# Optimization experiments

Measured on AMD Instinct MI355X. Metric: run time of the kernel, lower is better.

Reference implementation:

```python
import jax, jax.numpy as jnp
import numpy as np

NUM_USERS = 100000
NUM_ITEMS = 50000
DIM = 64
N_LAYERS = 3
L_W = 1e-4
E0 = 600000          # raw user-item interactions
B = 8192             # BPR batch size
N_NODES = NUM_USERS + NUM_ITEMS


def setup_inputs() -> dict:
    key = jax.random.key(0)
    k1, k2, k3, k4, k5, k6, k7 = jax.random.split(key, 7)
    return {
        "Gu": jax.random.normal(k1, (NUM_USERS, DIM), jnp.float32) * 0.1,
        "Gi": jax.random.normal(k2, (NUM_ITEMS, DIM), jnp.float32) * 0.1,
        "edge_user": jax.random.randint(k3, (E0,), 0, NUM_USERS),
        "edge_item": jax.random.randint(k4, (E0,), 0, NUM_ITEMS),
        "user": jax.random.randint(k5, (B,), 0, NUM_USERS),
        "pos": jax.random.randint(k6, (B,), 0, NUM_ITEMS),
        "neg": jax.random.randint(k7, (B,), 0, NUM_ITEMS),
    }


def _propagate(Gu, Gi, src, dst):
    # symmetric normalized adjacency (gcn_norm, no self-loops, as in LGConv)
    deg = jax.ops.segment_sum(jnp.ones_like(src, jnp.float32), dst,
                              num_segments=N_NODES)
    dinv = jnp.where(deg > 0, jax.lax.rsqrt(deg), 0.0)
    w = dinv[src] * dinv[dst]                      # [E]
    x = jnp.concatenate([Gu, Gi], axis=0)          # [N, D]
    acc = x
    h = x
    for _ in range(N_LAYERS):
        # SpMM: h' = D^-1/2 A D^-1/2 h  (gather + weighted scatter-add)
        h = jax.ops.segment_sum(w[:, None] * h[src], dst,
                                num_segments=N_NODES)
        acc = acc + h
    emb = acc / (N_LAYERS + 1)                     # mean over all layers
    return emb[:NUM_USERS], emb[NUM_USERS:]


def reference(Gu, Gi, edge_user, edge_item, user, pos, neg):
    # symmetrize bipartite edges; items offset by NUM_USERS
    src = jnp.concatenate([edge_user, edge_item + NUM_USERS])
    dst = jnp.concatenate([edge_item + NUM_USERS, edge_user])
    gu, gi = _propagate(Gu, Gi, src, dst)
    gu_u, gi_p, gi_n = gu[user], gi[pos], gi[neg]  # [B, D]
    xu_pos = jnp.sum(gu_u * gi_p, axis=1)
    xu_neg = jnp.sum(gu_u * gi_n, axis=1)
    mf_loss = -jnp.mean(jax.nn.log_sigmoid(xu_pos - xu_neg))
    reg = L_W * 0.5 * (jnp.sum(gu_u ** 2) + jnp.sum(gi_p ** 2)
                       + jnp.sum(gi_n ** 2)) / B
    return mf_loss + reg
```

## Files before the change

### kernel.cpp

```cpp
#include <hip/hip_runtime.h>

#define NUSERS 100000
#define NITEMS 50000
#define NNODES 150000
#define DIM 64
#define E0 600000
#define E2 (2 * E0)
#define BB 8192
#define LW 1e-4f
#define NN16 150016
#define LOSS_BLOCKS 512
#define SPMM_B 2344
#define SPMMB_B 384

#define NBUCK 1172
#define CHUNK_E 2048
#define CHUNKS 293
#define CPAD 320
#define BCAP 3072

__device__ __forceinline__ float bf_lo(unsigned u) { return __uint_as_float(u << 16); }
__device__ __forceinline__ float bf_hi(unsigned u) { return __uint_as_float(u & 0xffff0000u); }
__device__ __forceinline__ unsigned rne16(float x) {
  unsigned u = __float_as_uint(x);
  return (u + 0x7fffu + ((u >> 16) & 1u)) >> 16;
}
__device__ __forceinline__ unsigned pack2(float lo, float hi) {
  return rne16(lo) | (rne16(hi) << 16);
}

#define ACC8(X) do { \
    a0 += bf_lo((X).x); a1 += bf_hi((X).x); a2 += bf_lo((X).y); a3 += bf_hi((X).y); \
    a4 += bf_lo((X).z); a5 += bf_hi((X).z); a6 += bf_lo((X).w); a7 += bf_hi((X).w); \
  } while (0)

__global__ __launch_bounds__(256) void k_bcount(const int* __restrict__ eu,
                                                const int* __restrict__ ei,
                                                int* __restrict__ cnt) {
  __shared__ int h[NBUCK];
  for (int i = threadIdx.x; i < NBUCK; i += 256) h[i] = 0;
  __syncthreads();
  int c = blockIdx.x;
  int e0 = c * CHUNK_E;
  int e1 = min(e0 + CHUNK_E, E0);
  for (int e = e0 + threadIdx.x; e < e1; e += 256) {
    int u = eu[e];
    int it = NUSERS + ei[e];
    atomicAdd(&h[u >> 7], 1);
    atomicAdd(&h[it >> 7], 1);
  }
  __syncthreads();
  for (int i = threadIdx.x; i < NBUCK; i += 256) cnt[(size_t)i * CPAD + c] = h[i];
}

__global__ __launch_bounds__(256) void k_bscan1(int* __restrict__ cnt,
                                                int* __restrict__ btot) {
  int b = blockIdx.x * 4 + (threadIdx.x >> 6);
  int lane = threadIdx.x & 63;
  int* row = cnt + (size_t)b * CPAD;
  int carry = 0;
  for (int c0 = 0; c0 < CHUNKS; c0 += 64) {
    int c = c0 + lane;
    int v = (c < CHUNKS) ? row[c] : 0;
    int s = v;
    #pragma unroll
    for (int m = 1; m < 64; m <<= 1) {
      int t = __shfl_up(s, m);
      if (lane >= m) s += t;
    }
    if (c < CHUNKS) row[c] = carry + s - v;
    carry += __shfl(s, 63);
  }
  if (lane == 63) btot[b] = carry;
}

__global__ void k_bbase(const int* __restrict__ btot, int* __restrict__ bbase) {
  __shared__ int s[1024];
  int t = threadIdx.x;
  int i0 = 2 * t, i1 = 2 * t + 1;
  int v0 = (i0 < NBUCK) ? btot[i0] : 0;
  int v1 = (i1 < NBUCK) ? btot[i1] : 0;
  s[t] = v0 + v1;
  __syncthreads();
  for (int off = 1; off < 1024; off <<= 1) {
    int x = 0;
    if (t >= off) x = s[t - off];
    __syncthreads();
    if (t >= off) s[t] += x;
    __syncthreads();
  }
  int base = (t > 0) ? s[t - 1] : 0;
  if (i0 < NBUCK) bbase[i0] = base;
  if (i1 < NBUCK) bbase[i1] = base + v0;
}

__global__ __launch_bounds__(256) void k_bscatter(const int* __restrict__ eu,
                                                  const int* __restrict__ ei,
                                                  const int* __restrict__ cnt,
                                                  const int* __restrict__ bbase,
                                                  unsigned* __restrict__ pk) {
  __shared__ int soff[NBUCK];
  int c = blockIdx.x;
  for (int i = threadIdx.x; i < NBUCK; i += 256)
    soff[i] = cnt[(size_t)i * CPAD + c] + bbase[i];
  __syncthreads();
  int e0 = c * CHUNK_E;
  int e1 = min(e0 + CHUNK_E, E0);
  for (int e = e0 + threadIdx.x; e < e1; e += 256) {
    int u = eu[e];
    int it = NUSERS + ei[e];
    int s1 = atomicAdd(&soff[u >> 7], 1);
    pk[s1] = ((unsigned)it << 7) | (unsigned)(u & 127);
    int s2 = atomicAdd(&soff[it >> 7], 1);
    pk[s2] = ((unsigned)u << 7) | (unsigned)(it & 127);
  }
}

__global__ __launch_bounds__(256) void k_bucket_csr(
    const unsigned* __restrict__ pk, const int* __restrict__ btot,
    const int* __restrict__ bbase, int* __restrict__ deg, int* __restrict__ ptr,
    float* __restrict__ dinv, int* __restrict__ col,
    const float4* __restrict__ Gu4, const float4* __restrict__ Gi4,
    uint2* __restrict__ h0) {
  __shared__ unsigned sitm[BCAP];
  __shared__ int lcol[BCAP];
  __shared__ int ldeg[128], lscan[128], lcnt[128];
  __shared__ float sdv[128];
  int b = blockIdx.x;
  int base = bbase[b];
  int n = btot[b];
  for (int i = threadIdx.x; i < n; i += 256)
    if (i < BCAP) sitm[i] = pk[base + i];
  if (threadIdx.x < 128) { ldeg[threadIdx.x] = 0; lcnt[threadIdx.x] = 0; }
  __syncthreads();
  for (int i = threadIdx.x; i < n; i += 256) {
    unsigned p = (i < BCAP) ? sitm[i] : pk[base + i];
    atomicAdd(&ldeg[p & 127], 1);
  }
  __syncthreads();
  if (threadIdx.x < 128) lscan[threadIdx.x] = ldeg[threadIdx.x];
  __syncthreads();
  for (int off = 1; off < 128; off <<= 1) {
    int t = 0;
    if (threadIdx.x < 128 && (int)threadIdx.x >= off) t = lscan[threadIdx.x - off];
    __syncthreads();
    if (threadIdx.x < 128 && (int)threadIdx.x >= off) lscan[threadIdx.x] += t;
    __syncthreads();
  }
  int node = b * 128 + threadIdx.x;
  if (threadIdx.x < 128) {
    int d = ldeg[threadIdx.x];
    lscan[threadIdx.x] -= d;
    float dv = d > 0 ? rsqrtf((float)d) : 0.0f;
    sdv[threadIdx.x] = dv;
    if (node < NNODES) {
      deg[node] = d;
      ptr[node] = base + lscan[threadIdx.x];
      dinv[node] = dv;
    }
  }
  __syncthreads();
  for (int i = threadIdx.x; i < n; i += 256) {
    unsigned p = (i < BCAP) ? sitm[i] : pk[base + i];
    int dl = p & 127;
    int nb = (int)(p >> 7);
    int dnode = b * 128 + dl;
    int val = (dnode < NUSERS) ? nb - NUSERS : nb;
    int rel = lscan[dl] + atomicAdd(&lcnt[dl], 1);
    if (rel < BCAP) lcol[rel] = val;
    else col[base + rel] = val;
  }
  __syncthreads();
  int nf = min(n, BCAP);
  for (int i = threadIdx.x; i < nf; i += 256) col[base + i] = lcol[i];
  for (int w = threadIdx.x; w < 128 * 16; w += 256) {
    int nl = w >> 4, q = w & 15;
    int nd = b * 128 + nl;
    if (nd < NNODES) {
      float dv = sdv[nl];
      float4 v = (nd < NUSERS) ? Gu4[(size_t)nd * 16 + q]
                               : Gi4[(size_t)(nd - NUSERS) * 16 + q];
      h0[(size_t)nd * 16 + q] =
          make_uint2(pack2(dv * v.x, dv * v.y), pack2(dv * v.z, dv * v.w));
    }
  }
}

__global__ __launch_bounds__(512) void k_spmm2(
    const int* __restrict__ ptr, const int* __restrict__ deg,
    const int* __restrict__ col, const float* __restrict__ dinv,
    const uint4* __restrict__ h, uint4* __restrict__ hout) {
  int t = blockIdx.x * 512 + threadIdx.x;
  int g = t >> 3;
  int q = t & 7;
  if (g >= NNODES) return;
  const uint4* hq = ((g < NUSERS) ? h + (size_t)NUSERS * 8 : h) + q;
  int st = ptr[g], dg = deg[g];
  float dn = dinv[g];
  float a0 = 0, a1 = 0, a2 = 0, a3 = 0, a4 = 0, a5 = 0, a6 = 0, a7 = 0;
  int jend = st + dg;
  int j = st;
  for (; j + 4 <= jend; j += 4) {
    int c0 = col[j], c1 = col[j + 1], c2 = col[j + 2], c3 = col[j + 3];
    uint4 x0 = hq[(size_t)c0 * 8];
    uint4 x1 = hq[(size_t)c1 * 8];
    uint4 x2 = hq[(size_t)c2 * 8];
    uint4 x3 = hq[(size_t)c3 * 8];
    ACC8(x0); ACC8(x1); ACC8(x2); ACC8(x3);
  }
  if (j + 2 <= jend) {
    int c0 = col[j], c1 = col[j + 1];
    uint4 x0 = hq[(size_t)c0 * 8];
    uint4 x1 = hq[(size_t)c1 * 8];
    ACC8(x0); ACC8(x1);
    j += 2;
  }
  if (j < jend) {
    int c0 = col[j];
    uint4 x0 = hq[(size_t)c0 * 8];
    ACC8(x0);
  }
  float s = dn * dn;
  hout[(size_t)g * 8 + q] = make_uint4(pack2(a0 * s, a1 * s), pack2(a2 * s, a3 * s),
                                       pack2(a4 * s, a5 * s), pack2(a6 * s, a7 * s));
}

__device__ __forceinline__ int decode_node(int k, const int* __restrict__ usr,
                                           const int* __restrict__ pos,
                                           const int* __restrict__ neg, int* coff) {
  if (k < BB) { *coff = NUSERS; return usr[k]; }
  if (k < 2 * BB) { *coff = 0; return NUSERS + pos[k - BB]; }
  *coff = 0; return NUSERS + neg[k - 2 * BB];
}

__global__ __launch_bounds__(512) void k_spmm_batch(
    const int* __restrict__ usr, const int* __restrict__ pos, const int* __restrict__ neg,
    const int* __restrict__ ptr, const int* __restrict__ deg,
    const int* __restrict__ col, const float* __restrict__ dinv,
    const uint4* __restrict__ h, uint4* __restrict__ e3) {
  int t = blockIdx.x * 512 + threadIdx.x;
  int k = t >> 3;
  int q = t & 7;
  int coff;
  int g = decode_node(k, usr, pos, neg, &coff);
  const uint4* hq = h + (size_t)coff * 8 + q;
  int st = ptr[g], dg = deg[g];
  float dn = dinv[g];
  float a0 = 0, a1 = 0, a2 = 0, a3 = 0, a4 = 0, a5 = 0, a6 = 0, a7 = 0;
  int jend = st + dg;
  int j = st;
  for (; j + 4 <= jend; j += 4) {
    int c0 = col[j], c1 = col[j + 1], c2 = col[j + 2], c3 = col[j + 3];
    uint4 x0 = hq[(size_t)c0 * 8];
    uint4 x1 = hq[(size_t)c1 * 8];
    uint4 x2 = hq[(size_t)c2 * 8];
    uint4 x3 = hq[(size_t)c3 * 8];
    ACC8(x0); ACC8(x1); ACC8(x2); ACC8(x3);
  }
  if (j + 2 <= jend) {
    int c0 = col[j], c1 = col[j + 1];
    uint4 x0 = hq[(size_t)c0 * 8];
    uint4 x1 = hq[(size_t)c1 * 8];
    ACC8(x0); ACC8(x1);
    j += 2;
  }
  if (j < jend) {
    int c0 = col[j];
    uint4 x0 = hq[(size_t)c0 * 8];
    ACC8(x0);
  }
  float s = dn * dn;
  e3[(size_t)k * 8 + q] = make_uint4(pack2(a0 * s, a1 * s), pack2(a2 * s, a3 * s),
                                     pack2(a4 * s, a5 * s), pack2(a6 * s, a7 * s));
}

__global__ void k_loss(const int* __restrict__ usr, const int* __restrict__ pos,
                       const int* __restrict__ neg, const int* __restrict__ deg,
                       const float4* __restrict__ Gu4, const float4* __restrict__ Gi4,
                       const uint2* __restrict__ h1, const uint2* __restrict__ h2,
                       const uint2* __restrict__ e3, float* __restrict__ bpart) {
  __shared__ float sL[4], sR[4];
  int wid = threadIdx.x >> 6;
  int lane = threadIdx.x & 63;
  int r = lane >> 4;
  int q = lane & 15;
  int gw = blockIdx.x * 4 + wid;
  int nw = gridDim.x * 4;
  const float s = 0.25f;
  float accL = 0.0f, accR = 0.0f;
  for (int b4 = gw; b4 < BB / 4; b4 += nw) {
    int b = b4 * 4 + r;
    int iu = usr[b], ip = pos[b], ig = neg[b];
    float sdu = sqrtf((float)deg[iu]);
    float sdp = sqrtf((float)deg[NUSERS + ip]);
    float sdn = sqrtf((float)deg[NUSERS + ig]);
    size_t ou = (size_t)iu * 16 + q;
    size_t op = ((size_t)NUSERS + ip) * 16 + q;
    size_t on = ((size_t)NUSERS + ig) * 16 + q;
    float4 u = Gu4[ou];
    float4 p = Gi4[(size_t)ip * 16 + q];
    float4 g = Gi4[(size_t)ig * 16 + q];
    float4 su = {0, 0, 0, 0}, sp = {0, 0, 0, 0}, sg = {0, 0, 0, 0};
    uint2 v;
    v = h1[ou]; su.x += bf_lo(v.x); su.y += bf_hi(v.x); su.z += bf_lo(v.y); su.w += bf_hi(v.y);
    v = h2[ou]; su.x += bf_lo(v.x); su.y += bf_hi(v.x); su.z += bf_lo(v.y); su.w += bf_hi(v.y);
    v = e3[(size_t)b * 16 + q];
    su.x += bf_lo(v.x); su.y += bf_hi(v.x); su.z += bf_lo(v.y); su.w += bf_hi(v.y);
    v = h1[op]; sp.x += bf_lo(v.x); sp.y += bf_hi(v.x); sp.z += bf_lo(v.y); sp.w += bf_hi(v.y);
    v = h2[op]; sp.x += bf_lo(v.x); sp.y += bf_hi(v.x); sp.z += bf_lo(v.y); sp.w += bf_hi(v.y);
    v = e3[((size_t)BB + b) * 16 + q];
    sp.x += bf_lo(v.x); sp.y += bf_hi(v.x); sp.z += bf_lo(v.y); sp.w += bf_hi(v.y);
    v = h1[on]; sg.x += bf_lo(v.x); sg.y += bf_hi(v.x); sg.z += bf_lo(v.y); sg.w += bf_hi(v.y);
    v = h2[on]; sg.x += bf_lo(v.x); sg.y += bf_hi(v.x); sg.z += bf_lo(v.y); sg.w += bf_hi(v.y);
    v = e3[((size_t)2 * BB + b) * 16 + q];
    sg.x += bf_lo(v.x); sg.y += bf_hi(v.x); sg.z += bf_lo(v.y); sg.w += bf_hi(v.y);
    u.x = (u.x + sdu * su.x) * s; u.y = (u.y + sdu * su.y) * s;
    u.z = (u.z + sdu * su.z) * s; u.w = (u.w + sdu * su.w) * s;
    p.x = (p.x + sdp * sp.x) * s; p.y = (p.y + sdp * sp.y) * s;
    p.z = (p.z + sdp * sp.z) * s; p.w = (p.w + sdp * sp.w) * s;
    g.x = (g.x + sdn * sg.x) * s; g.y = (g.y + sdn * sg.y) * s;
    g.z = (g.z + sdn * sg.z) * s; g.w = (g.w + sdn * sg.w) * s;
    float dp = u.x * p.x + u.y * p.y + u.z * p.z + u.w * p.w;
    float dn = u.x * g.x + u.y * g.y + u.z * g.z + u.w * g.w;
    float rg = u.x * u.x + u.y * u.y + u.z * u.z + u.w * u.w
             + p.x * p.x + p.y * p.y + p.z * p.z + p.w * p.w
             + g.x * g.x + g.y * g.y + g.z * g.z + g.w * g.w;
    #pragma unroll
    for (int m = 1; m <= 8; m <<= 1) {
      dp += __shfl_xor(dp, m);
      dn += __shfl_xor(dn, m);
      rg += __shfl_xor(rg, m);
    }
    if (q == 0) {
      float diff = dp - dn;
      accL -= fminf(diff, 0.0f) - log1pf(expf(-fabsf(diff)));
      accR += rg;
    }
  }
  accL += __shfl_xor(accL, 16); accR += __shfl_xor(accR, 16);
  accL += __shfl_xor(accL, 32); accR += __shfl_xor(accR, 32);
  if (lane == 0) { sL[wid] = accL; sR[wid] = accR; }
  __syncthreads();
  if (threadIdx.x == 0) {
    bpart[blockIdx.x] = sL[0] + sL[1] + sL[2] + sL[3];
    bpart[LOSS_BLOCKS + blockIdx.x] = sR[0] + sR[1] + sR[2] + sR[3];
  }
}

__global__ void k_final(const float* __restrict__ bpart, float* __restrict__ out) {
  int lane = threadIdx.x;
  float l = 0.0f, r = 0.0f;
  #pragma unroll
  for (int i = 0; i < LOSS_BLOCKS; i += 64) {
    l += bpart[lane + i];
    r += bpart[LOSS_BLOCKS + lane + i];
  }
  for (int off = 32; off > 0; off >>= 1) {
    l += __shfl_down(l, off);
    r += __shfl_down(r, off);
  }
  if (lane == 0) out[0] = l * (1.0f / BB) + LW * 0.5f * r * (1.0f / BB);
}

extern "C" void kernel_launch(void* const* d_in, const int* in_sizes, int n_in,
                              void* d_out, int out_size, void* d_ws, size_t ws_size,
                              hipStream_t stream) {
  const float* Gu = (const float*)d_in[0];
  const float* Gi = (const float*)d_in[1];
  const int* eu  = (const int*)d_in[2];
  const int* ei  = (const int*)d_in[3];
  const int* usr = (const int*)d_in[4];
  const int* pos = (const int*)d_in[5];
  const int* neg = (const int*)d_in[6];
  float* out = (float*)d_out;

  int* deg    = (int*)d_ws;
  int* ptr    = deg + NN16;
  float* dinv = (float*)(ptr + NN16);
  int* col    = (int*)(dinv + NN16);
  uint2* h0   = (uint2*)(col + E2);
  uint2* h1   = h0 + (size_t)NNODES * 16;
  uint2* h2   = h1 + (size_t)NNODES * 16;
  uint2* h3   = h2 + (size_t)NNODES * 16;
  float* bpart = (float*)(h3 + (size_t)NNODES * 16);

  unsigned* pk = (unsigned*)h1;
  int* cnt     = (int*)h2;
  int* btot    = (int*)h3;
  int* bbase   = btot + 1280;

  const float4* Gu4 = (const float4*)Gu;
  const float4* Gi4 = (const float4*)Gi;

  k_bcount<<<CHUNKS, 256, 0, stream>>>(eu, ei, cnt);
  k_bscan1<<<NBUCK / 4, 256, 0, stream>>>(cnt, btot);
  k_bbase<<<1, 1024, 0, stream>>>(btot, bbase);
  k_bscatter<<<CHUNKS, 256, 0, stream>>>(eu, ei, cnt, bbase, pk);
  k_bucket_csr<<<NBUCK, 256, 0, stream>>>(pk, btot, bbase, deg, ptr, dinv, col,
                                          Gu4, Gi4, h0);

  k_spmm2<<<SPMM_B, 512, 0, stream>>>(ptr, deg, col, dinv,
                                      (const uint4*)h0, (uint4*)h1);
  k_spmm2<<<SPMM_B, 512, 0, stream>>>(ptr, deg, col, dinv,
                                      (const uint4*)h1, (uint4*)h2);
  k_spmm_batch<<<SPMMB_B, 512, 0, stream>>>(usr, pos, neg, ptr, deg, col, dinv,
                                            (const uint4*)h2, (uint4*)h3);

  k_loss<<<LOSS_BLOCKS, 256, 0, stream>>>(usr, pos, neg, deg, Gu4, Gi4, h1, h2,
                                          (const uint2*)h3, bpart);
  k_final<<<1, 64, 0, stream>>>(bpart, out);
}
```

Baseline: 197.1 us.

## Fuse bucket-base scan into scatter and final SpMM layer into loss

Each scatter block now redundantly computes the exclusive scan of bucket totals in shared memory, so the single-block k_bbase kernel is gone. The batch-only third propagation layer is computed inside the loss kernel: each block builds the layer-3 rows for its 16 samples in shared memory instead of writing them to global memory for a separate kernel. This removes two kernel launches and the global round trip of the layer-3 embeddings. The cost is repeated scan work in every scatter block and lower parallelism in the gather phase of the loss kernel.

```diff
diff --git a/kernel.cpp b/kernel.cpp
--- a/kernel.cpp
+++ b/kernel.cpp
@@ -9,9 +9,8 @@
 #define BB 8192
 #define LW 1e-4f
 #define NN16 150016
-#define LOSS_BLOCKS 512
 #define SPMM_B 2344
-#define SPMMB_B 384
+#define LOSS3_B 512
 
 #define NBUCK 1172
 #define CHUNK_E 2048
@@ -32,6 +31,40 @@
 #define ACC8(X) do { \
     a0 += bf_lo((X).x); a1 += bf_hi((X).x); a2 += bf_lo((X).y); a3 += bf_hi((X).y); \
     a4 += bf_lo((X).z); a5 += bf_hi((X).z); a6 += bf_lo((X).w); a7 += bf_hi((X).w); \
+  } while (0)
+
+#define SPMM_BODY(COLP, HQ, DSTP, DSTIDX)                                    \
+  do {                                                                       \
+    const int dsti_ = (DSTIDX);                                              \
+    float a0 = 0, a1 = 0, a2 = 0, a3 = 0, a4 = 0, a5 = 0, a6 = 0, a7 = 0;    \
+    int jend_ = st + dg;                                                     \
+    int j_ = st;                                                             \
+    for (; j_ + 4 <= jend_; j_ += 4) {                                       \
+      int c0_ = (COLP)[j_], c1_ = (COLP)[j_ + 1];                            \
+      int c2_ = (COLP)[j_ + 2], c3_ = (COLP)[j_ + 3];                        \
+      uint4 x0_ = (HQ)[(size_t)c0_ * 8];                                     \
+      uint4 x1_ = (HQ)[(size_t)c1_ * 8];                                     \
+      uint4 x2_ = (HQ)[(size_t)c2_ * 8];                                     \
+      uint4 x3_ = (HQ)[(size_t)c3_ * 8];                                     \
+      ACC8(x0_); ACC8(x1_); ACC8(x2_); ACC8(x3_);                            \
+    }                                                                        \
+    if (j_ + 2 <= jend_) {                                                   \
+      int c0_ = (COLP)[j_], c1_ = (COLP)[j_ + 1];                            \
+      uint4 x0_ = (HQ)[(size_t)c0_ * 8];                                     \
+      uint4 x1_ = (HQ)[(size_t)c1_ * 8];                                     \
+      ACC8(x0_); ACC8(x1_);                                                  \
+      j_ += 2;                                                               \
+    }                                                                        \
+    if (j_ < jend_) {                                                        \
+      int c0_ = (COLP)[j_];                                                  \
+      uint4 x0_ = (HQ)[(size_t)c0_ * 8];                                     \
+      ACC8(x0_);                                                             \
+    }                                                                        \
+    float scl_ = dn * dn;                                                    \
+    (DSTP)[dsti_] = make_uint4(pack2(a0 * scl_, a1 * scl_),                  \
+                               pack2(a2 * scl_, a3 * scl_),                  \
+                               pack2(a4 * scl_, a5 * scl_),                  \
+                               pack2(a6 * scl_, a7 * scl_));                 \
   } while (0)
 
 __global__ __launch_bounds__(256) void k_bcount(const int* __restrict__ eu,
@@ -74,44 +107,45 @@
   if (lane == 63) btot[b] = carry;
 }
 
-__global__ void k_bbase(const int* __restrict__ btot, int* __restrict__ bbase) {
-  __shared__ int s[1024];
-  int t = threadIdx.x;
-  int i0 = 2 * t, i1 = 2 * t + 1;
-  int v0 = (i0 < NBUCK) ? btot[i0] : 0;
-  int v1 = (i1 < NBUCK) ? btot[i1] : 0;
-  s[t] = v0 + v1;
-  __syncthreads();
-  for (int off = 1; off < 1024; off <<= 1) {
-    int x = 0;
-    if (t >= off) x = s[t - off];
-    __syncthreads();
-    if (t >= off) s[t] += x;
-    __syncthreads();
-  }
-  int base = (t > 0) ? s[t - 1] : 0;
-  if (i0 < NBUCK) bbase[i0] = base;
-  if (i1 < NBUCK) bbase[i1] = base + v0;
-}
-
 __global__ __launch_bounds__(256) void k_bscatter(const int* __restrict__ eu,
                                                   const int* __restrict__ ei,
                                                   const int* __restrict__ cnt,
-                                                  const int* __restrict__ bbase,
+                                                  const int* __restrict__ btot,
+                                                  int* __restrict__ bbase,
                                                   unsigned* __restrict__ pk) {
-  __shared__ int soff[NBUCK];
-  int c = blockIdx.x;
-  for (int i = threadIdx.x; i < NBUCK; i += 256)
-    soff[i] = cnt[(size_t)i * CPAD + c] + bbase[i];
-  __syncthreads();
-  int e0 = c * CHUNK_E;
-  int e1 = min(e0 + CHUNK_E, E0);
-  for (int e = e0 + threadIdx.x; e < e1; e += 256) {
+  __shared__ int S[1280];
+  __shared__ int T[256];
+  int bid = blockIdx.x, tid = threadIdx.x;
+  for (int i = tid; i < 1280; i += 256) S[i] = (i < NBUCK) ? btot[i] : 0;
+  __syncthreads();
+  int b0 = tid * 5;
+  int run = 0;
+  #pragma unroll
+  for (int k = 0; k < 5; k++) { run += S[b0 + k]; S[b0 + k] = run; }
+  T[tid] = run;
+  __syncthreads();
+  for (int off = 1; off < 256; off <<= 1) {
+    int t = 0;
+    if (tid >= off) t = T[tid - off];
+    __syncthreads();
+    if (tid >= off) T[tid] += t;
+    __syncthreads();
+  }
+  int texc = T[tid] - run;
+  for (int k = 4; k >= 0; k--)
+    S[b0 + k] = texc + (k ? S[b0 + k - 1] : 0);
+  if (bid == 0)
+    for (int i = tid; i < NBUCK; i += 256) bbase[i] = S[i];
+  __syncthreads();
+  for (int i = tid; i < NBUCK; i += 256) S[i] += cnt[(size_t)i * CPAD + bid];
+  __syncthreads();
+  int e0 = bid * CHUNK_E, e1 = min(e0 + CHUNK_E, E0);
+  for (int e = e0 + tid; e < e1; e += 256) {
     int u = eu[e];
     int it = NUSERS + ei[e];
-    int s1 = atomicAdd(&soff[u >> 7], 1);
+    int s1 = atomicAdd(&S[u >> 7], 1);
     pk[s1] = ((unsigned)it << 7) | (unsigned)(u & 127);
-    int s2 = atomicAdd(&soff[it >> 7], 1);
+    int s2 = atomicAdd(&S[it >> 7], 1);
     pk[s2] = ((unsigned)u << 7) | (unsigned)(it & 127);
   }
 }
@@ -197,153 +231,95 @@
   const uint4* hq = ((g < NUSERS) ? h + (size_t)NUSERS * 8 : h) + q;
   int st = ptr[g], dg = deg[g];
   float dn = dinv[g];
-  float a0 = 0, a1 = 0, a2 = 0, a3 = 0, a4 = 0, a5 = 0, a6 = 0, a7 = 0;
-  int jend = st + dg;
-  int j = st;
-  for (; j + 4 <= jend; j += 4) {
-    int c0 = col[j], c1 = col[j + 1], c2 = col[j + 2], c3 = col[j + 3];
-    uint4 x0 = hq[(size_t)c0 * 8];
-    uint4 x1 = hq[(size_t)c1 * 8];
-    uint4 x2 = hq[(size_t)c2 * 8];
-    uint4 x3 = hq[(size_t)c3 * 8];
-    ACC8(x0); ACC8(x1); ACC8(x2); ACC8(x3);
-  }
-  if (j + 2 <= jend) {
-    int c0 = col[j], c1 = col[j + 1];
-    uint4 x0 = hq[(size_t)c0 * 8];
-    uint4 x1 = hq[(size_t)c1 * 8];
-    ACC8(x0); ACC8(x1);
-    j += 2;
-  }
-  if (j < jend) {
-    int c0 = col[j];
-    uint4 x0 = hq[(size_t)c0 * 8];
-    ACC8(x0);
-  }
-  float s = dn * dn;
-  hout[(size_t)g * 8 + q] = make_uint4(pack2(a0 * s, a1 * s), pack2(a2 * s, a3 * s),
-                                       pack2(a4 * s, a5 * s), pack2(a6 * s, a7 * s));
-}
-
-__device__ __forceinline__ int decode_node(int k, const int* __restrict__ usr,
-                                           const int* __restrict__ pos,
-                                           const int* __restrict__ neg, int* coff) {
-  if (k < BB) { *coff = NUSERS; return usr[k]; }
-  if (k < 2 * BB) { *coff = 0; return NUSERS + pos[k - BB]; }
-  *coff = 0; return NUSERS + neg[k - 2 * BB];
-}
-
-__global__ __launch_bounds__(512) void k_spmm_batch(
-    const int* __restrict__ usr, const int* __restrict__ pos, const int* __restrict__ neg,
-    const int* __restrict__ ptr, const int* __restrict__ deg,
-    const int* __restrict__ col, const float* __restrict__ dinv,
-    const uint4* __restrict__ h, uint4* __restrict__ e3) {
-  int t = blockIdx.x * 512 + threadIdx.x;
-  int k = t >> 3;
-  int q = t & 7;
-  int coff;
-  int g = decode_node(k, usr, pos, neg, &coff);
-  const uint4* hq = h + (size_t)coff * 8 + q;
-  int st = ptr[g], dg = deg[g];
-  float dn = dinv[g];
-  float a0 = 0, a1 = 0, a2 = 0, a3 = 0, a4 = 0, a5 = 0, a6 = 0, a7 = 0;
-  int jend = st + dg;
-  int j = st;
-  for (; j + 4 <= jend; j += 4) {
-    int c0 = col[j], c1 = col[j + 1], c2 = col[j + 2], c3 = col[j + 3];
-    uint4 x0 = hq[(size_t)c0 * 8];
-    uint4 x1 = hq[(size_t)c1 * 8];
-    uint4 x2 = hq[(size_t)c2 * 8];
-    uint4 x3 = hq[(size_t)c3 * 8];
-    ACC8(x0); ACC8(x1); ACC8(x2); ACC8(x3);
-  }
-  if (j + 2 <= jend) {
-    int c0 = col[j], c1 = col[j + 1];
-    uint4 x0 = hq[(size_t)c0 * 8];
-    uint4 x1 = hq[(size_t)c1 * 8];
-    ACC8(x0); ACC8(x1);
-    j += 2;
-  }
-  if (j < jend) {
-    int c0 = col[j];
-    uint4 x0 = hq[(size_t)c0 * 8];
-    ACC8(x0);
-  }
-  float s = dn * dn;
-  e3[(size_t)k * 8 + q] = make_uint4(pack2(a0 * s, a1 * s), pack2(a2 * s, a3 * s),
-                                     pack2(a4 * s, a5 * s), pack2(a6 * s, a7 * s));
-}
-
-__global__ void k_loss(const int* __restrict__ usr, const int* __restrict__ pos,
-                       const int* __restrict__ neg, const int* __restrict__ deg,
-                       const float4* __restrict__ Gu4, const float4* __restrict__ Gi4,
-                       const uint2* __restrict__ h1, const uint2* __restrict__ h2,
-                       const uint2* __restrict__ e3, float* __restrict__ bpart) {
+  SPMM_BODY(col, hq, hout, (size_t)g * 8 + q);
+}
+
+__global__ __launch_bounds__(256) void k_loss3(
+    const int* __restrict__ usr, const int* __restrict__ pos,
+    const int* __restrict__ neg, const int* __restrict__ ptr,
+    const int* __restrict__ deg, const int* __restrict__ col,
+    const float* __restrict__ dinv,
+    const float4* __restrict__ Gu4, const float4* __restrict__ Gi4,
+    const uint4* __restrict__ h2v, const uint2* __restrict__ h1u,
+    const uint2* __restrict__ h2u, float* __restrict__ bpart) {
+  __shared__ uint4 sh3[48 * 8];
   __shared__ float sL[4], sR[4];
-  int wid = threadIdx.x >> 6;
-  int lane = threadIdx.x & 63;
-  int r = lane >> 4;
-  int q = lane & 15;
-  int gw = blockIdx.x * 4 + wid;
-  int nw = gridDim.x * 4;
-  const float s = 0.25f;
+  int bid = blockIdx.x, tid = threadIdx.x;
+
+  for (int t = tid; t < 48 * 8; t += 256) {
+    int s = t >> 3, q = t & 7;
+    int bb = s / 3, role = s - bb * 3;
+    int b = bid * 16 + bb;
+    int g, coff;
+    if (role == 0) { g = usr[b]; coff = NUSERS; }
+    else if (role == 1) { g = NUSERS + pos[b]; coff = 0; }
+    else { g = NUSERS + neg[b]; coff = 0; }
+    const uint4* hq = h2v + (size_t)coff * 8 + q;
+    int st = ptr[g], dg = deg[g];
+    float dn = dinv[g];
+    SPMM_BODY(col, hq, sh3, s * 8 + q);
+  }
+  __syncthreads();
+
+  const uint2* sh3u = (const uint2*)sh3;
+  int wid = tid >> 6, lane = tid & 63;
+  int bb = tid >> 4, q = tid & 15;
+  int b = bid * 16 + bb;
+  const float sc = 0.25f;
+  int iu = usr[b], ip = pos[b], ig = neg[b];
+  float sdu = sqrtf((float)deg[iu]);
+  float sdp = sqrtf((float)deg[NUSERS + ip]);
+  float sdn = sqrtf((float)deg[NUSERS + ig]);
+  size_t ou = (size_t)iu * 16 + q;
+  size_t op = ((size_t)NUSERS + ip) * 16 + q;
+  size_t on = ((size_t)NUSERS + ig) * 16 + q;
+  float4 u = Gu4[ou];
+  float4 p = Gi4[(size_t)ip * 16 + q];
+  float4 g = Gi4[(size_t)ig * 16 + q];
+  float4 su = {0, 0, 0, 0}, sp = {0, 0, 0, 0}, sg = {0, 0, 0, 0};
+  uint2 v;
+  v = h1u[ou]; su.x += bf_lo(v.x); su.y += bf_hi(v.x); su.z += bf_lo(v.y); su.w += bf_hi(v.y);
+  v = h2u[ou]; su.x += bf_lo(v.x); su.y += bf_hi(v.x); su.z += bf_lo(v.y); su.w += bf_hi(v.y);
+  v = sh3u[(size_t)(bb * 3 + 0) * 16 + q];
+  su.x += bf_lo(v.x); su.y += bf_hi(v.x); su.z += bf_lo(v.y); su.w += bf_hi(v.y);
+  v = h1u[op]; sp.x += bf_lo(v.x); sp.y += bf_hi(v.x); sp.z += bf_lo(v.y); sp.w += bf_hi(v.y);
+  v = h2u[op]; sp.x += bf_lo(v.x); sp.y += bf_hi(v.x); sp.z += bf_lo(v.y); sp.w += bf_hi(v.y);
+  v = sh3u[(size_t)(bb * 3 + 1) * 16 + q];
+  sp.x += bf_lo(v.x); sp.y += bf_hi(v.x); sp.z += bf_lo(v.y); sp.w += bf_hi(v.y);
+  v = h1u[on]; sg.x += bf_lo(v.x); sg.y += bf_hi(v.x); sg.z += bf_lo(v.y); sg.w += bf_hi(v.y);
+  v = h2u[on]; sg.x += bf_lo(v.x); sg.y += bf_hi(v.x); sg.z += bf_lo(v.y); sg.w += bf_hi(v.y);
+  v = sh3u[(size_t)(bb * 3 + 2) * 16 + q];
+  sg.x += bf_lo(v.x); sg.y += bf_hi(v.x); sg.z += bf_lo(v.y); sg.w += bf_hi(v.y);
+  u.x = (u.x + sdu * su.x) * sc; u.y = (u.y + sdu * su.y) * sc;
+  u.z = (u.z + sdu * su.z) * sc; u.w = (u.w + sdu * su.w) * sc;
+  p.x = (p.x + sdp * sp.x) * sc; p.y = (p.y + sdp * sp.y) * sc;
+  p.z = (p.z + sdp * sp.z) * sc; p.w = (p.w + sdp * sp.w) * sc;
+  g.x = (g.x + sdn * sg.x) * sc; g.y = (g.y + sdn * sg.y) * sc;
+  g.z = (g.z + sdn * sg.z) * sc; g.w = (g.w + sdn * sg.w) * sc;
+  float dp = u.x * p.x + u.y * p.y + u.z * p.z + u.w * p.w;
+  float dn = u.x * g.x + u.y * g.y + u.z * g.z + u.w * g.w;
+  float rg = u.x * u.x + u.y * u.y + u.z * u.z + u.w * u.w
+           + p.x * p.x + p.y * p.y + p.z * p.z + p.w * p.w
+           + g.x * g.x + g.y * g.y + g.z * g.z + g.w * g.w;
+  #pragma unroll
+  for (int m = 1; m <= 8; m <<= 1) {
+    dp += __shfl_xor(dp, m);
+    dn += __shfl_xor(dn, m);
+    rg += __shfl_xor(rg, m);
+  }
   float accL = 0.0f, accR = 0.0f;
-  for (int b4 = gw; b4 < BB / 4; b4 += nw) {
-    int b = b4 * 4 + r;
-    int iu = usr[b], ip = pos[b], ig = neg[b];
-    float sdu = sqrtf((float)deg[iu]);
-    float sdp = sqrtf((float)deg[NUSERS + ip]);
-    float sdn = sqrtf((float)deg[NUSERS + ig]);
-    size_t ou = (size_t)iu * 16 + q;
-    size_t op = ((size_t)NUSERS + ip) * 16 + q;
-    size_t on = ((size_t)NUSERS + ig) * 16 + q;
-    float4 u = Gu4[ou];
-    float4 p = Gi4[(size_t)ip * 16 + q];
-    float4 g = Gi4[(size_t)ig * 16 + q];
-    float4 su = {0, 0, 0, 0}, sp = {0, 0, 0, 0}, sg = {0, 0, 0, 0};
-    uint2 v;
-    v = h1[ou]; su.x += bf_lo(v.x); su.y += bf_hi(v.x); su.z += bf_lo(v.y); su.w += bf_hi(v.y);
-    v = h2[ou]; su.x += bf_lo(v.x); su.y += bf_hi(v.x); su.z += bf_lo(v.y); su.w += bf_hi(v.y);
-    v = e3[(size_t)b * 16 + q];
-    su.x += bf_lo(v.x); su.y += bf_hi(v.x); su.z += bf_lo(v.y); su.w += bf_hi(v.y);
-    v = h1[op]; sp.x += bf_lo(v.x); sp.y += bf_hi(v.x); sp.z += bf_lo(v.y); sp.w += bf_hi(v.y);
-    v = h2[op]; sp.x += bf_lo(v.x); sp.y += bf_hi(v.x); sp.z += bf_lo(v.y); sp.w += bf_hi(v.y);
-    v = e3[((size_t)BB + b) * 16 + q];
-    sp.x += bf_lo(v.x); sp.y += bf_hi(v.x); sp.z += bf_lo(v.y); sp.w += bf_hi(v.y);
-    v = h1[on]; sg.x += bf_lo(v.x); sg.y += bf_hi(v.x); sg.z += bf_lo(v.y); sg.w += bf_hi(v.y);
-    v = h2[on]; sg.x += bf_lo(v.x); sg.y += bf_hi(v.x); sg.z += bf_lo(v.y); sg.w += bf_hi(v.y);
-    v = e3[((size_t)2 * BB + b) * 16 + q];
-    sg.x += bf_lo(v.x); sg.y += bf_hi(v.x); sg.z += bf_lo(v.y); sg.w += bf_hi(v.y);
-    u.x = (u.x + sdu * su.x) * s; u.y = (u.y + sdu * su.y) * s;
-    u.z = (u.z + sdu * su.z) * s; u.w = (u.w + sdu * su.w) * s;
-    p.x = (p.x + sdp * sp.x) * s; p.y = (p.y + sdp * sp.y) * s;
-    p.z = (p.z + sdp * sp.z) * s; p.w = (p.w + sdp * sp.w) * s;
-    g.x = (g.x + sdn * sg.x) * s; g.y = (g.y + sdn * sg.y) * s;
-    g.z = (g.z + sdn * sg.z) * s; g.w = (g.w + sdn * sg.w) * s;
-    float dp = u.x * p.x + u.y * p.y + u.z * p.z + u.w * p.w;
-    float dn = u.x * g.x + u.y * g.y + u.z * g.z + u.w * g.w;
-    float rg = u.x * u.x + u.y * u.y + u.z * u.z + u.w * u.w
-             + p.x * p.x + p.y * p.y + p.z * p.z + p.w * p.w
-             + g.x * g.x + g.y * g.y + g.z * g.z + g.w * g.w;
-    #pragma unroll
-    for (int m = 1; m <= 8; m <<= 1) {
-      dp += __shfl_xor(dp, m);
-      dn += __shfl_xor(dn, m);
-      rg += __shfl_xor(rg, m);
-    }
-    if (q == 0) {
-      float diff = dp - dn;
-      accL -= fminf(diff, 0.0f) - log1pf(expf(-fabsf(diff)));
-      accR += rg;
-    }
+  if (q == 0) {
+    float diff = dp - dn;
+    accL = -(fminf(diff, 0.0f) - log1pf(expf(-fabsf(diff))));
+    accR = rg;
   }
   accL += __shfl_xor(accL, 16); accR += __shfl_xor(accR, 16);
   accL += __shfl_xor(accL, 32); accR += __shfl_xor(accR, 32);
   if (lane == 0) { sL[wid] = accL; sR[wid] = accR; }
   __syncthreads();
-  if (threadIdx.x == 0) {
-    bpart[blockIdx.x] = sL[0] + sL[1] + sL[2] + sL[3];
-    bpart[LOSS_BLOCKS + blockIdx.x] = sR[0] + sR[1] + sR[2] + sR[3];
+  if (tid == 0) {
+    bpart[bid] = sL[0] + sL[1] + sL[2] + sL[3];
+    bpart[LOSS3_B + bid] = sR[0] + sR[1] + sR[2] + sR[3];
   }
 }
 
@@ -351,9 +327,9 @@
   int lane = threadIdx.x;
   float l = 0.0f, r = 0.0f;
   #pragma unroll
-  for (int i = 0; i < LOSS_BLOCKS; i += 64) {
+  for (int i = 0; i < LOSS3_B; i += 64) {
     l += bpart[lane + i];
-    r += bpart[LOSS_BLOCKS + lane + i];
+    r += bpart[LOSS3_B + lane + i];
   }
   for (int off = 32; off > 0; off >>= 1) {
     l += __shfl_down(l, off);
@@ -393,9 +369,8 @@
   const float4* Gi4 = (const float4*)Gi;
 
   k_bcount<<<CHUNKS, 256, 0, stream>>>(eu, ei, cnt);
-  k_bscan1<<<NBUCK / 4, 256, 0, stream>>>(cnt, btot);
-  k_bbase<<<1, 1024, 0, stream>>>(btot, bbase);
-  k_bscatter<<<CHUNKS, 256, 0, stream>>>(eu, ei, cnt, bbase, pk);
+  k_bscan1<<<CHUNKS, 256, 0, stream>>>(cnt, btot);
+  k_bscatter<<<CHUNKS, 256, 0, stream>>>(eu, ei, cnt, btot, bbase, pk);
   k_bucket_csr<<<NBUCK, 256, 0, stream>>>(pk, btot, bbase, deg, ptr, dinv, col,
                                           Gu4, Gi4, h0);
 
@@ -403,10 +378,9 @@
                                       (const uint4*)h0, (uint4*)h1);
   k_spmm2<<<SPMM_B, 512, 0, stream>>>(ptr, deg, col, dinv,
                                       (const uint4*)h1, (uint4*)h2);
-  k_spmm_batch<<<SPMMB_B, 512, 0, stream>>>(usr, pos, neg, ptr, deg, col, dinv,
-                                            (const uint4*)h2, (uint4*)h3);
-
-  k_loss<<<LOSS_BLOCKS, 256, 0, stream>>>(usr, pos, neg, deg, Gu4, Gi4, h1, h2,
-                                          (const uint2*)h3, bpart);
+
+  k_loss3<<<LOSS3_B, 256, 0, stream>>>(usr, pos, neg, ptr, deg, col, dinv,
+                                       Gu4, Gi4, (const uint4*)h2,
+                                       (const uint2*)h1, (const uint2*)h2, bpart);
   k_final<<<1, 64, 0, stream>>>(bpart, out);
 }
```

Result: no change. 198.1 us (+0.5%).
